# Kernel optimization log

Hardware: AMD Instinct MI355X
Metric: run time of the kernel (lower is better)

## Reference

```python
import jax, jax.numpy as jnp
import numpy as np


def setup_inputs() -> dict:
    key = jax.random.key(0)
    ks = jax.random.split(key, 4)
    B, C, H, W = 8, 256, 64, 64
    Cq = C // 8
    x = jax.random.normal(ks[0], (B, C, H, W), dtype=jnp.float32)
    wq = jax.random.normal(ks[1], (Cq, C), dtype=jnp.float32) * (1.0 / np.sqrt(C))
    bq = jnp.zeros((Cq,), dtype=jnp.float32)
    wk = jax.random.normal(ks[2], (Cq, C), dtype=jnp.float32) * (1.0 / np.sqrt(C))
    bk = jnp.zeros((Cq,), dtype=jnp.float32)
    wv = jax.random.normal(ks[3], (C, C), dtype=jnp.float32) * (1.0 / np.sqrt(C))
    bv = jnp.zeros((C,), dtype=jnp.float32)
    return {"x": x, "wq": wq, "bq": bq, "wk": wk, "bk": bk, "wv": wv, "bv": bv}


def reference(x, wq, bq, wk, bk, wv, bv):
    B, C, H, W = x.shape
    N = H * W
    xf = x.reshape(B, C, N)  # [B, C, N] ; 1x1 conv == channel matmul
    q = jnp.einsum('bcn,dc->bnd', xf, wq) + bq          # [B, N, Cq]
    k = jnp.einsum('bcn,dc->bdn', xf, wk) + bk[:, None]  # [B, Cq, N]
    v = jnp.einsum('bcn,dc->bdn', xf, wv) + bv[:, None]  # [B, C, N]
    energy = jnp.einsum('bnd,bdm->bnm', q, k)           # [B, N, N]
    attn = jax.nn.softmax(energy, axis=-1)              # softmax over keys
    # out[b,c,i] = sum_j v[b,c,j] * attn[b,i,j]
    out = jnp.einsum('bcj,bij->bci', v, attn).reshape(B, C, H, W)
    return x + out
```

## Files before the change

kernel.cpp:

```cpp
#include <hip/hip_runtime.h>


#define CH  256
#define DQ  32
#define NSP 4096
#define RWS 320

typedef short short8 __attribute__((ext_vector_type(8)));
typedef float float4v __attribute__((ext_vector_type(4)));

__device__ __forceinline__ unsigned short f2b(float f) {
  unsigned int u = __float_as_uint(f);
  unsigned int r = u + 0x7fffu + ((u >> 16) & 1u);
  return (unsigned short)(r >> 16);
}
__device__ __forceinline__ short8 ld8(const unsigned short* p) {
  return *(const short8*)p;
}

__global__ __launch_bounds__(256) void prep_kernel(
    const float* __restrict__ wq, const float* __restrict__ bq,
    const float* __restrict__ wk, const float* __restrict__ bk,
    const float* __restrict__ wv, const float* __restrict__ bv,
    unsigned short* __restrict__ wh, unsigned short* __restrict__ wl,
    float* __restrict__ ball) {
  int r = blockIdx.x, c = threadIdx.x;
  float v;
  if (r < 32)       v = wq[r * CH + c];
  else if (r < 64)  v = wk[(r - 32) * CH + c];
  else              v = wv[(r - 64) * CH + c];
  unsigned int u = __float_as_uint(v);
  unsigned short hi = (unsigned short)(u >> 16);
  float hf = __uint_as_float(u & 0xffff0000u);
  unsigned short lo = (unsigned short)(__float_as_uint(v - hf) >> 16);
  wh[r * CH + c] = hi;
  wl[r * CH + c] = lo;
  if (c == 0)
    ball[r] = (r < 32) ? bq[r] : (r < 64 ? bk[r - 32] : bv[r - 64]);
}

__global__ __launch_bounds__(256, 2) void proj_kernel(
    const float* __restrict__ x,
    const unsigned short* __restrict__ wh, const unsigned short* __restrict__ wl,
    const float* __restrict__ ball,
    unsigned short* __restrict__ qb, unsigned short* __restrict__ kb,
    unsigned short* __restrict__ vb, int b0) {
  const int bz   = blockIdx.z;
  const int bg   = b0 + bz;
  const int n0   = blockIdx.x * 64;
  const int t    = threadIdx.x;
  const int w    = t >> 6;
  const int lane = t & 63;
  const int col  = lane & 15;
  const int quad = lane >> 4;
  const int r0   = 80 * w;

  const float* xb = x + (size_t)bg * CH * NSP;

  float4v acc[5][4];
#pragma unroll
  for (int rf = 0; rf < 5; ++rf) {
    float bias = ball[r0 + 16 * rf + col];
#pragma unroll
    for (int ns = 0; ns < 4; ++ns)
      acc[rf][ns] = (float4v){bias, bias, bias, bias};
  }

  float xv[4][8];
#pragma unroll
  for (int ns = 0; ns < 4; ++ns)
#pragma unroll
    for (int j = 0; j < 8; ++j)
      xv[ns][j] = xb[(size_t)(quad * 8 + j) * NSP + n0 + ns * 16 + col];

#pragma unroll 1
  for (int ks = 0; ks < 8; ++ks) {
    const int k0 = ks * 32;
    short8 wfh[5], wfl[5];
#pragma unroll
    for (int rf = 0; rf < 5; ++rf) {
      size_t wo = (size_t)(r0 + 16 * rf + col) * CH + k0 + quad * 8;
      wfh[rf] = ld8(wh + wo);
      wfl[rf] = ld8(wl + wo);
    }
    short8 ah[4], al[4];
#pragma unroll
    for (int ns = 0; ns < 4; ++ns)
#pragma unroll
      for (int j = 0; j < 8; ++j) {
        float v = xv[ns][j];
        unsigned int u = __float_as_uint(v);
        ah[ns][j] = (short)(u >> 16);
        float hf = __uint_as_float(u & 0xffff0000u);
        al[ns][j] = (short)(__float_as_uint(v - hf) >> 16);
      }
    if (ks < 7) {
#pragma unroll
      for (int ns = 0; ns < 4; ++ns)
#pragma unroll
        for (int j = 0; j < 8; ++j)
          xv[ns][j] = xb[(size_t)(k0 + 32 + quad * 8 + j) * NSP + n0 + ns * 16 + col];
    }
#pragma unroll
    for (int rf = 0; rf < 5; ++rf)
#pragma unroll
      for (int ns = 0; ns < 4; ++ns) {
        acc[rf][ns] = __builtin_amdgcn_mfma_f32_16x16x32_bf16(ah[ns], wfh[rf], acc[rf][ns], 0, 0, 0);
        acc[rf][ns] = __builtin_amdgcn_mfma_f32_16x16x32_bf16(al[ns], wfh[rf], acc[rf][ns], 0, 0, 0);
        acc[rf][ns] = __builtin_amdgcn_mfma_f32_16x16x32_bf16(ah[ns], wfl[rf], acc[rf][ns], 0, 0, 0);
      }
  }

#pragma unroll
  for (int rf = 0; rf < 5; ++rf) {
    const int rr = r0 + 16 * rf + col;
    const int rb = r0 + 16 * rf;
#pragma unroll
    for (int ns = 0; ns < 4; ++ns) {
      const int nb = n0 + ns * 16 + quad * 4;
      if (rb < 32) {
#pragma unroll
        for (int reg = 0; reg < 4; ++reg)
          qb[((size_t)bz * NSP + nb + reg) * DQ + rr] = f2b(acc[rf][ns][reg]);
      } else if (rb < 64) {
#pragma unroll
        for (int reg = 0; reg < 4; ++reg)
          kb[((size_t)bz * NSP + nb + reg) * DQ + (rr - 32)] = f2b(acc[rf][ns][reg]);
      } else {
        ushort4 o = {f2b(acc[rf][ns][0]), f2b(acc[rf][ns][1]),
                     f2b(acc[rf][ns][2]), f2b(acc[rf][ns][3])};
        *(ushort4*)&vb[((size_t)bz * CH + (rr - 64)) * NSP + nb] = o;
      }
    }
  }
}

__global__ __launch_bounds__(512, 4) void attn_kernel(
    const float* __restrict__ x,
    const unsigned short* __restrict__ qb, const unsigned short* __restrict__ kb,
    const unsigned short* __restrict__ vb,
    float* __restrict__ out, int b0, int ns) {
  __shared__ unsigned short ps[2][64][72];
  __shared__ float buf[4][64];
  __shared__ float lf[64];

  const int bl   = blockIdx.x % ns;
  const int bg   = b0 + bl;
  const int i0   = (blockIdx.x / ns) * 64;
  const int t    = threadIdx.x;
  const int w    = t >> 6;
  const int rh   = w >> 2;
  const int kq   = w & 3;
  const int lane = t & 63;
  const int col  = lane & 15;
  const int quad = lane >> 4;
  const float LOG2E = 1.4426950408889634f;

  const unsigned short* qbb = qb + (size_t)bl * NSP * DQ;
  const unsigned short* kbb = kb + (size_t)bl * NSP * DQ;
  const unsigned short* vbb = vb + (size_t)bl * CH * NSP;

  short8 qf[2];
#pragma unroll
  for (int rgp = 0; rgp < 2; ++rgp)
    qf[rgp] = ld8(qbb + (size_t)(i0 + 32 * rh + 16 * rgp + col) * DQ + quad * 8);
  const float4v z4 = (float4v){0.f, 0.f, 0.f, 0.f};

  float m_[2][4];
#pragma unroll
  for (int rgp = 0; rgp < 2; ++rgp)
#pragma unroll
    for (int reg = 0; reg < 4; ++reg) m_[rgp][reg] = -3.0e38f;

  short8 kf = ld8(kbb + (size_t)(16 * kq + col) * DQ + quad * 8);
  for (int j0 = 0; j0 < NSP; j0 += 64) {
    int jn = (j0 + 64 < NSP) ? j0 + 64 : 0;
    short8 kfn = ld8(kbb + (size_t)(jn + 16 * kq + col) * DQ + quad * 8);
    float4v c0 = __builtin_amdgcn_mfma_f32_16x16x32_bf16(qf[0], kf, z4, 0, 0, 0);
    float4v c1 = __builtin_amdgcn_mfma_f32_16x16x32_bf16(qf[1], kf, z4, 0, 0, 0);
#pragma unroll
    for (int reg = 0; reg < 4; ++reg) {
      m_[0][reg] = fmaxf(m_[0][reg], c0[reg]);
      m_[1][reg] = fmaxf(m_[1][reg], c1[reg]);
    }
    kf = kfn;
  }
#pragma unroll
  for (int rgp = 0; rgp < 2; ++rgp)
#pragma unroll
    for (int reg = 0; reg < 4; ++reg) {
#pragma unroll
      for (int mask = 1; mask <= 8; mask <<= 1)
        m_[rgp][reg] = fmaxf(m_[rgp][reg], __shfl_xor(m_[rgp][reg], mask));
    }
  if (col == 0) {
#pragma unroll
    for (int rgp = 0; rgp < 2; ++rgp)
#pragma unroll
      for (int reg = 0; reg < 4; ++reg)
        buf[kq][32 * rh + 16 * rgp + quad * 4 + reg] = m_[rgp][reg];
  }
  __syncthreads();
  float moff[2][4];
#pragma unroll
  for (int rgp = 0; rgp < 2; ++rgp)
#pragma unroll
    for (int reg = 0; reg < 4; ++reg) {
      int row = 32 * rh + 16 * rgp + quad * 4 + reg;
      float m = fmaxf(fmaxf(buf[0][row], buf[1][row]),
                      fmaxf(buf[2][row], buf[3][row]));
      moff[rgp][reg] = m * LOG2E;
    }
  __syncthreads();

  float4v acc[4][2];
#pragma unroll
  for (int rg = 0; rg < 4; ++rg)
#pragma unroll
    for (int ct = 0; ct < 2; ++ct) acc[rg][ct] = z4;
  float lp[2][4];
#pragma unroll
  for (int rgp = 0; rgp < 2; ++rgp)
#pragma unroll
    for (int reg = 0; reg < 4; ++reg) lp[rgp][reg] = 0.0f;

  kf = ld8(kbb + (size_t)(16 * kq + col) * DQ + quad * 8);
  for (int j0 = 0; j0 < NSP; j0 += 64) {
    const int cp = (j0 >> 6) & 1;
    short8 vf[2][2];
#pragma unroll
    for (int ct = 0; ct < 2; ++ct)
#pragma unroll
      for (int h = 0; h < 2; ++h)
        vf[ct][h] = ld8(vbb + (size_t)(32 * w + 16 * ct + col) * NSP
                        + j0 + 32 * h + quad * 8);
    float4v c0 = __builtin_amdgcn_mfma_f32_16x16x32_bf16(qf[0], kf, z4, 0, 0, 0);
    float4v c1 = __builtin_amdgcn_mfma_f32_16x16x32_bf16(qf[1], kf, z4, 0, 0, 0);
    int jn = (j0 + 64 < NSP) ? j0 + 64 : 0;
    short8 kfn = ld8(kbb + (size_t)(jn + 16 * kq + col) * DQ + quad * 8);
#pragma unroll
    for (int reg = 0; reg < 4; ++reg) {
      float p0 = __builtin_amdgcn_exp2f(fmaf(c0[reg], LOG2E, -moff[0][reg]));
      float p1 = __builtin_amdgcn_exp2f(fmaf(c1[reg], LOG2E, -moff[1][reg]));
      lp[0][reg] += p0;
      lp[1][reg] += p1;
      ps[cp][32 * rh + quad * 4 + reg][16 * kq + col]      = f2b(p0);
      ps[cp][32 * rh + 16 + quad * 4 + reg][16 * kq + col] = f2b(p1);
    }
    __syncthreads();

#pragma unroll
    for (int rg = 0; rg < 4; ++rg) {
      short8 pf0 = *(const short8*)&ps[cp][16 * rg + col][quad * 8];
      short8 pf1 = *(const short8*)&ps[cp][16 * rg + col][32 + quad * 8];
#pragma unroll
      for (int ct = 0; ct < 2; ++ct) {
        acc[rg][ct] = __builtin_amdgcn_mfma_f32_16x16x32_bf16(pf0, vf[ct][0], acc[rg][ct], 0, 0, 0);
        acc[rg][ct] = __builtin_amdgcn_mfma_f32_16x16x32_bf16(pf1, vf[ct][1], acc[rg][ct], 0, 0, 0);
      }
    }
    kf = kfn;
  }

#pragma unroll
  for (int rgp = 0; rgp < 2; ++rgp)
#pragma unroll
    for (int reg = 0; reg < 4; ++reg) {
#pragma unroll
      for (int mask = 1; mask <= 8; mask <<= 1)
        lp[rgp][reg] += __shfl_xor(lp[rgp][reg], mask);
    }
  if (col == 0) {
#pragma unroll
    for (int rgp = 0; rgp < 2; ++rgp)
#pragma unroll
      for (int reg = 0; reg < 4; ++reg)
        buf[kq][32 * rh + 16 * rgp + quad * 4 + reg] = lp[rgp][reg];
  }
  __syncthreads();
  if (kq == 0 && col == 0) {
#pragma unroll
    for (int rgp = 0; rgp < 2; ++rgp)
#pragma unroll
      for (int reg = 0; reg < 4; ++reg) {
        int row = 32 * rh + 16 * rgp + quad * 4 + reg;
        lf[row] = 1.0f / (buf[0][row] + buf[1][row] + buf[2][row] + buf[3][row]);
      }
  }
  __syncthreads();

#pragma unroll
  for (int rg = 0; rg < 4; ++rg) {
    float linv[4];
#pragma unroll
    for (int reg = 0; reg < 4; ++reg)
      linv[reg] = lf[16 * rg + quad * 4 + reg];
#pragma unroll
    for (int ct = 0; ct < 2; ++ct) {
      int c  = 32 * w + 16 * ct + col;
      int ib = i0 + 16 * rg + quad * 4;
      size_t idx = ((size_t)bg * CH + c) * NSP + ib;
      float4 xr = *(const float4*)&x[idx];
      float4 o;
      o.x = acc[rg][ct][0] * linv[0] + xr.x;
      o.y = acc[rg][ct][1] * linv[1] + xr.y;
      o.z = acc[rg][ct][2] * linv[2] + xr.z;
      o.w = acc[rg][ct][3] * linv[3] + xr.w;
      *(float4*)&out[idx] = o;
    }
  }
}

extern "C" void kernel_launch(void* const* d_in, const int* in_sizes, int n_in,
                              void* d_out, int out_size, void* d_ws, size_t ws_size,
                              hipStream_t stream) {
  (void)in_sizes; (void)n_in; (void)out_size;
  const float* x  = (const float*)d_in[0];
  const float* wq = (const float*)d_in[1];
  const float* bq = (const float*)d_in[2];
  const float* wk = (const float*)d_in[3];
  const float* bk = (const float*)d_in[4];
  const float* wv = (const float*)d_in[5];
  const float* bv = (const float*)d_in[6];
  float* out = (float*)d_out;

  const size_t WALL_B = (size_t)RWS * CH * sizeof(float) + 4096;
  const size_t QB_B = (size_t)NSP * DQ * sizeof(unsigned short);
  const size_t VB_B = (size_t)CH * NSP * sizeof(unsigned short);
  const size_t PER_B = 2 * QB_B + VB_B;

  int ns = 8;
  while (ns > 1 && WALL_B + (size_t)ns * PER_B > ws_size) ns >>= 1;

  char* ws = (char*)d_ws;
  unsigned short* wh = (unsigned short*)ws;
  unsigned short* wl = wh + (size_t)RWS * CH;
  float* ball = (float*)(ws + (size_t)RWS * CH * 2 * sizeof(unsigned short));
  char* qkv = ws + WALL_B;
  unsigned short* qb = (unsigned short*)qkv;
  unsigned short* kb = (unsigned short*)(qkv + (size_t)ns * QB_B);
  unsigned short* vb = (unsigned short*)(qkv + (size_t)ns * 2 * QB_B);

  prep_kernel<<<dim3(RWS), dim3(256), 0, stream>>>(wq, bq, wk, bk, wv, bv, wh, wl, ball);
  for (int b0 = 0; b0 < 8; b0 += ns) {
    proj_kernel<<<dim3(64, 1, ns), dim3(256), 0, stream>>>(
        x, wh, wl, ball, qb, kb, vb, b0);
    attn_kernel<<<dim3(64 * ns), dim3(512), 0, stream>>>(
        x, qb, kb, vb, out, b0, ns);
  }
}
```

Baseline: 268.0 us.

## Stage x tiles via async global-to-LDS loads and swizzle P buffer layout

```diff
diff --git a/kernel.cpp b/kernel.cpp
--- a/kernel.cpp
+++ b/kernel.cpp
@@ -39,12 +39,30 @@
     ball[r] = (r < 32) ? bq[r] : (r < 64 ? bk[r - 32] : bv[r - 64]);
 }
 
+__device__ __forceinline__ void stage_x(const float* xkn, float* buf,
+                                        int w, int lane) {
+#pragma unroll
+  for (int i = 0; i < 2; ++i) {
+    const int h  = 2 * w + i;
+    const int sw = ((h >> 1) & 1) * 16;
+    const int c  = h * 4 + (lane >> 4);
+    const int n  = ((lane & 15) * 4) ^ sw;
+    const float* gp = xkn + (size_t)c * NSP + n;
+    __builtin_amdgcn_global_load_lds(
+        (const __attribute__((address_space(1))) unsigned int*)gp,
+        (__attribute__((address_space(3))) unsigned int*)(buf + h * 256),
+        16, 0, 0);
+  }
+}
+
 __global__ __launch_bounds__(256, 2) void proj_kernel(
     const float* __restrict__ x,
     const unsigned short* __restrict__ wh, const unsigned short* __restrict__ wl,
     const float* __restrict__ ball,
     unsigned short* __restrict__ qb, unsigned short* __restrict__ kb,
     unsigned short* __restrict__ vb, int b0) {
+  __shared__ float xs[2][2048];
+
   const int bz   = blockIdx.z;
   const int bg   = b0 + bz;
   const int n0   = blockIdx.x * 64;
@@ -54,6 +72,8 @@
   const int col  = lane & 15;
   const int quad = lane >> 4;
   const int r0   = 80 * w;
+  const int e    = (quad & 1) * 16;
+  const int lbase = quad * 512 + col;
 
   const float* xb = x + (size_t)bg * CH * NSP;
 
@@ -66,16 +86,16 @@
       acc[rf][ns] = (float4v){bias, bias, bias, bias};
   }
 
-  float xv[4][8];
-#pragma unroll
-  for (int ns = 0; ns < 4; ++ns)
-#pragma unroll
-    for (int j = 0; j < 8; ++j)
-      xv[ns][j] = xb[(size_t)(quad * 8 + j) * NSP + n0 + ns * 16 + col];
+  stage_x(xb + n0, xs[0], w, lane);
+  __syncthreads();
+  int cur = 0;
 
 #pragma unroll 1
   for (int ks = 0; ks < 8; ++ks) {
     const int k0 = ks * 32;
+    if (ks < 7)
+      stage_x(xb + (size_t)(k0 + 32) * NSP + n0, xs[cur ^ 1], w, lane);
+
     short8 wfh[5], wfl[5];
 #pragma unroll
     for (int rf = 0; rf < 5; ++rf) {
@@ -83,24 +103,22 @@
       wfh[rf] = ld8(wh + wo);
       wfl[rf] = ld8(wl + wo);
     }
+
+    const float* xc = &xs[cur][0];
     short8 ah[4], al[4];
 #pragma unroll
-    for (int ns = 0; ns < 4; ++ns)
+    for (int nsb = 0; nsb < 4; ++nsb) {
+      const float* xp2 = xc + lbase + ((nsb * 16) ^ e);
 #pragma unroll
       for (int j = 0; j < 8; ++j) {
-        float v = xv[ns][j];
+        float v = xp2[j * 64];
         unsigned int u = __float_as_uint(v);
-        ah[ns][j] = (short)(u >> 16);
+        ah[nsb][j] = (short)(u >> 16);
         float hf = __uint_as_float(u & 0xffff0000u);
-        al[ns][j] = (short)(__float_as_uint(v - hf) >> 16);
-      }
-    if (ks < 7) {
-#pragma unroll
-      for (int ns = 0; ns < 4; ++ns)
-#pragma unroll
-        for (int j = 0; j < 8; ++j)
-          xv[ns][j] = xb[(size_t)(k0 + 32 + quad * 8 + j) * NSP + n0 + ns * 16 + col];
-    }
+        al[nsb][j] = (short)(__float_as_uint(v - hf) >> 16);
+      }
+    }
+
 #pragma unroll
     for (int rf = 0; rf < 5; ++rf)
 #pragma unroll
@@ -109,6 +127,9 @@
         acc[rf][ns] = __builtin_amdgcn_mfma_f32_16x16x32_bf16(al[ns], wfh[rf], acc[rf][ns], 0, 0, 0);
         acc[rf][ns] = __builtin_amdgcn_mfma_f32_16x16x32_bf16(ah[ns], wfl[rf], acc[rf][ns], 0, 0, 0);
       }
+
+    __syncthreads();
+    cur ^= 1;
   }
 
 #pragma unroll
@@ -140,7 +161,7 @@
     const unsigned short* __restrict__ qb, const unsigned short* __restrict__ kb,
     const unsigned short* __restrict__ vb,
     float* __restrict__ out, int b0, int ns) {
-  __shared__ unsigned short ps[2][64][72];
+  __shared__ unsigned short ps[2 * 64 * 64];
   __shared__ float buf[4][64];
   __shared__ float lf[64];
 
@@ -166,6 +187,11 @@
     qf[rgp] = ld8(qbb + (size_t)(i0 + 32 * rh + 16 * rgp + col) * DQ + quad * 8);
   const float4v z4 = (float4v){0.f, 0.f, 0.f, 0.f};
 
+  const int kb8 = 2 * kq + (col >> 3);
+  const int ci  = col & 7;
+  const int q4  = 4 * (quad & 1);
+  const int ob  = quad ^ ci;
+
   float m_[2][4];
 #pragma unroll
   for (int rgp = 0; rgp < 2; ++rgp)
@@ -238,21 +264,25 @@
     float4v c1 = __builtin_amdgcn_mfma_f32_16x16x32_bf16(qf[1], kf, z4, 0, 0, 0);
     int jn = (j0 + 64 < NSP) ? j0 + 64 : 0;
     short8 kfn = ld8(kbb + (size_t)(jn + 16 * kq + col) * DQ + quad * 8);
+    unsigned short* pw = &ps[cp * 4096 + (32 * rh + quad * 4) * 64 + ci];
 #pragma unroll
     for (int reg = 0; reg < 4; ++reg) {
       float p0 = __builtin_amdgcn_exp2f(fmaf(c0[reg], LOG2E, -moff[0][reg]));
       float p1 = __builtin_amdgcn_exp2f(fmaf(c1[reg], LOG2E, -moff[1][reg]));
       lp[0][reg] += p0;
       lp[1][reg] += p1;
-      ps[cp][32 * rh + quad * 4 + reg][16 * kq + col]      = f2b(p0);
-      ps[cp][32 * rh + 16 + quad * 4 + reg][16 * kq + col] = f2b(p1);
+      const int so = reg * 64 + (kb8 ^ (q4 + reg)) * 8;
+      pw[so]        = f2b(p0);
+      pw[so + 1024] = f2b(p1);
     }
     __syncthreads();
 
+    const short8* pb0 = (const short8*)&ps[cp * 4096 + col * 64 + ob * 8];
+    const short8* pb1 = (const short8*)&ps[cp * 4096 + col * 64 + (ob ^ 4) * 8];
 #pragma unroll
     for (int rg = 0; rg < 4; ++rg) {
-      short8 pf0 = *(const short8*)&ps[cp][16 * rg + col][quad * 8];
-      short8 pf1 = *(const short8*)&ps[cp][16 * rg + col][32 + quad * 8];
+      short8 pf0 = pb0[rg * 128];
+      short8 pf1 = pb1[rg * 128];
 #pragma unroll
       for (int ct = 0; ct < 2; ++ct) {
         acc[rg][ct] = __builtin_amdgcn_mfma_f32_16x16x32_bf16(pf0, vf[ct][0], acc[rg][ct], 0, 0, 0);
```

Result: no change. 268.0 us (-0.0%).
